# Kernel tuning notes

Measured on AMD Instinct MI355X. Metric: run time of the kernel, lower is better.

The kernel has to match this reference:

```python
import jax, jax.numpy as jnp
import numpy as np

B, S, D, E = 4, 1024, 1024, 4
HID = 2816  # multiple_of * ceil(int(2*4*D/3) / multiple_of), multiple_of=256
COND = 1024  # min(D, 1024)
NORM_EPS = 1e-5  # block norms
LN_EPS = 1e-5    # q_norm/k_norm default eps


def setup_inputs() -> dict:
    key = jax.random.key(0)
    ks = jax.random.split(key, 16)
    w = lambda i, shape: jax.random.normal(ks[i], shape, jnp.float32) * 0.02
    return {
        'x': jax.random.normal(ks[0], (B, S, D), jnp.float32),
        'freqs_cis': jax.random.normal(ks[1], (S, 32), jnp.float32),  # unused by the block
        'adaln_input': jax.random.normal(ks[2], (B, COND), jnp.float32),
        'wq': w(3, (D, D)), 'wk': w(4, (D, D)), 'wv': w(5, (D, D)), 'wo': w(6, (D, D)),
        'q_norm_w': jnp.ones((D,), jnp.float32), 'q_norm_b': jnp.zeros((D,), jnp.float32),
        'k_norm_w': jnp.ones((D,), jnp.float32), 'k_norm_b': jnp.zeros((D,), jnp.float32),
        'attn_norm_w': jnp.ones((D,), jnp.float32), 'attn_norm_b': jnp.zeros((D,), jnp.float32),
        'ffn_norm_w': jnp.ones((D,), jnp.float32), 'ffn_norm_b': jnp.zeros((D,), jnp.float32),
        'w1': w(7, (E, D, HID)), 'w2': w(8, (E, HID, D)), 'w3': w(9, (E, D, HID)),
        'router_w': w(10, (D, E)), 'router_b': jnp.zeros((E,), jnp.float32),
        'ada_w': w(11, (COND, 6 * D)), 'ada_b': jnp.zeros((6 * D,), jnp.float32),
    }


def _ln(x, w, b, eps):
    mu = jnp.mean(x, -1, keepdims=True)
    var = jnp.mean((x - mu) ** 2, -1, keepdims=True)
    return (x - mu) * jax.lax.rsqrt(var + eps) * w + b


def _attention(x, wq, wk, wv, wo, qn_w, qn_b, kn_w, kn_b):
    # NOTE: this module attends over the FEATURE dim (no head split, no 1/sqrt(d) scale):
    # xq,xk,xv are permuted to [B, D, S]; scores are [B, D, D].
    q = _ln(x @ wq, qn_w, qn_b, LN_EPS)
    k = _ln(x @ wk, kn_w, kn_b, LN_EPS)
    v = x @ wv
    scores = jnp.einsum('bsd,bse->bde', q, k)          # [B, D, D]
    attn = jax.nn.softmax(scores, axis=-1)
    out = jnp.einsum('bde,bse->bsd', attn, v)          # [B, S, D]
    return out @ wo


def _moe(x, w1, w2, w3, router_w, router_b):
    logits = x @ router_w + router_b                   # [B, S, E]
    # F.normalize default dim=1 -> L2-normalize along the SEQUENCE dim (faithful quirk)
    nrm = jnp.sqrt(jnp.sum(logits * logits, axis=1, keepdims=True))
    logits = logits / jnp.maximum(nrm, 1e-12)
    probs = jax.nn.softmax(logits, axis=-1)
    topw, topi = jax.lax.top_k(probs, 2)
    # dense combine weights [B,S,E]: identical math to the masked gather/scatter dispatch
    combine = jnp.sum(jax.nn.one_hot(topi, E, dtype=x.dtype) * topw[..., None], axis=-2)
    h1 = jnp.einsum('bsd,edh->ebsh', x, w1)
    h3 = jnp.einsum('bsd,edh->ebsh', x, w3)
    out_e = jnp.einsum('ebsh,ehd->ebsd', jnp.sin(h1) * h3, w2)
    moe = jnp.einsum('bse,ebsd->bsd', combine, out_e)
    avg = jnp.mean(probs, axis=0)                      # [S, E] (mean over batch dim only)
    aux = jnp.sum((1.0 / E - avg) ** 2)
    return moe, aux


def reference(x, freqs_cis, adaln_input, wq, wk, wv, wo, q_norm_w, q_norm_b, k_norm_w,
              k_norm_b, attn_norm_w, attn_norm_b, ffn_norm_w, ffn_norm_b, w1, w2, w3,
              router_w, router_b, ada_w, ada_b):
    ada = jax.nn.silu(adaln_input) @ ada_w + ada_b     # [B, 6D]
    shift_msa, scale_msa, gate_msa, shift_mlp, scale_mlp, gate_mlp = jnp.split(ada, 6, axis=1)
    h = _ln(x, attn_norm_w, attn_norm_b, NORM_EPS)
    h = h * (1.0 + scale_msa[:, None, :]) + shift_msa[:, None, :]
    x = x + gate_msa[:, None, :] * _attention(h, wq, wk, wv, wo, q_norm_w, q_norm_b, k_norm_w, k_norm_b)
    h = _ln(x, ffn_norm_w, ffn_norm_b, NORM_EPS)
    h = h * (1.0 + scale_mlp[:, None, :]) + shift_mlp[:, None, :]
    # MoE path REPLACES x (no residual, gate_mlp unused) — faithful to the source
    x, aux = _moe(h, w1, w2, w3, router_w, router_b)
    return x, aux
```

## Files before the change

### kernel.cpp

```cpp
#include <hip/hip_runtime.h>
#include <hip/hip_bf16.h>
#include <math.h>

#define BB 4
#define SS 1024
#define DD 1024
#define EE 4
#define HID 2816
#define HC 1408
#define SIXD 6144
#define NSLOT 8704
#define NMB 68

typedef __bf16 v8bf __attribute__((ext_vector_type(8)));
typedef float  v4f  __attribute__((ext_vector_type(4)));

__device__ __forceinline__ ushort f2bf(float f) {
    union { float f; unsigned u; } v; v.f = f;
    unsigned r = v.u + 0x7fff + ((v.u >> 16) & 1);
    return (ushort)(r >> 16);
}
__device__ __forceinline__ float bf2f(ushort u) {
    union { unsigned u; float f; } v; v.u = ((unsigned)u) << 16;
    return v.f;
}
__device__ __forceinline__ void split_bf(float x, ushort& h, ushort& l) {
    h = f2bf(x);
    l = f2bf(x - bf2f(h));
}
__device__ __forceinline__ void gload16(const void* g, void* l) {
    __builtin_amdgcn_global_load_lds((const __attribute__((address_space(1))) void*)g,
                                     (__attribute__((address_space(3))) void*)l, 16, 0, 0);
}
template<int N> __device__ __forceinline__ void wait_vm() {
    __builtin_amdgcn_s_waitcnt((N & 15) | (0x7 << 4) | (0xF << 8) | ((N >> 4) << 14));
}

__device__ __forceinline__ void xcd_remap(int& bx, int& by) {
    const int gx = gridDim.x, gy = gridDim.y;
    const int nwg = gx * gy;
    const int wid = bx + gx * by;
    const int q = nwg >> 3, r = nwg & 7;
    const int xcd = wid & 7, loc = wid >> 3;
    const int pos = (xcd < r) ? (xcd * (q + 1) + loc)
                              : (r * (q + 1) + (xcd - r) * q + loc);
    bx = pos % gx; by = pos / gx;
}

__device__ __forceinline__ void xcd_remap_cm(int& bx, int& by) {
    const int gx = gridDim.x, gy = gridDim.y;
    const int nwg = gx * gy;
    const int wid = bx + gx * by;
    const int q = nwg >> 3, r = nwg & 7;
    const int xcd = wid & 7, loc = wid >> 3;
    const int pos = (xcd < r) ? (xcd * (q + 1) + loc)
                              : (r * (q + 1) + (xcd - r) * q + loc);
    bx = pos / gy; by = pos % gy;
}

__device__ __forceinline__ void moe_remap(int& bx, int& by) {
    const int gx = gridDim.x, gy = gridDim.y;
    const int total = gx * gy;
    const int wid = bx + gx * by;
    if ((total & 7) || (gx & 1)) { xcd_remap(bx, by); return; }
    const int q = total >> 3;
    const int pos = (wid & 7) * q + (wid >> 3);
    const int NG = gx >> 1;
    const int gh = NG * gy;
    const int nh = pos / gh, r = pos % gh;
    by = r / NG;
    bx = nh * NG + (r % NG);
}

template<int EPI, bool SPLIT, bool MOE>
__global__ __launch_bounds__(256, 2) void mgemm(
    const ushort* __restrict__ Ah, const ushort* __restrict__ Al,
    const ushort* __restrict__ Bh, const ushort* __restrict__ Bl,
    void* __restrict__ Cv, ushort* __restrict__ C2,
    const float* __restrict__ f1, const float* __restrict__ f2,
    const int* __restrict__ tokidx, const int* __restrict__ mbe,
    const int* __restrict__ mbm,
    int K, int lda, int ldb, int ldc,
    long sA, long sB, long sC)
{
    constexpr int STG = SPLIT ? 12288 : 6144;
    constexpr int BH  = SPLIT ? 8192 : 4096;
    constexpr int L   = SPLIT ? 6 : 3;
    __shared__ __align__(16) ushort smem[3 * STG];

    const int tid  = threadIdx.x;
    const int wv   = tid >> 6, lane = tid & 63;

    int bx = blockIdx.x, by = blockIdx.y;
    if (MOE) moe_remap(bx, by); else xcd_remap(bx, by);
    const int n0 = bx * 64;

    int eexp = 0, m0;
    if (MOE) {
        eexp = mbe[by];
        if (eexp < 0) return;
        m0 = mbm[by];
    } else {
        m0 = by * 128;
    }
    const long zA = MOE ? 0 : (long)blockIdx.z * sA;
    const long zB = MOE ? (long)eexp * sB : (long)blockIdx.z * sB;
    const long zC = MOE ? 0 : (long)blockIdx.z * sC;

    const int lrow = tid >> 2;
    const int skq  = ((tid & 3) ^ ((tid >> 3) & 3)) * 8;
    const int lm   = lane & 15;
    const int qs   = (((lane >> 4) ^ ((lm >> 1) & 3)) * 8);

    v4f acc[2][4];
    const v4f vzero = {0.f, 0.f, 0.f, 0.f};
    #pragma unroll
    for (int i = 0; i < 2; ++i)
        #pragma unroll
        for (int j = 0; j < 4; ++j) acc[i][j] = vzero;

    auto issue = [&](int kt, int st) {
        const long kk = (long)kt * 32 + skq;
        ushort* base = smem + st * STG;
        #pragma unroll
        for (int c = 0; c < 2; ++c) {
            const int row  = c * 64 + lrow;
            const int loff = (c * 64 + wv * 16) * 32;
            gload16(Ah + zA + (long)(m0 + row) * lda + kk, base + loff);
            if (SPLIT)
                gload16(Al + zA + (long)(m0 + row) * lda + kk, base + 4096 + loff);
        }
        {
            const int loff = wv * 16 * 32;
            gload16(Bh + zB + (long)(n0 + lrow) * ldb + kk, base + BH + loff);
            if (SPLIT)
                gload16(Bl + zB + (long)(n0 + lrow) * ldb + kk, base + BH + 2048 + loff);
        }
    };

    const int nk = K / 32;
    issue(0, 0);
    if (nk > 1) issue(1, 1);
    for (int kt = 0; kt < nk; ++kt) {
        if (kt + 1 < nk) wait_vm<L>(); else wait_vm<0>();
        __builtin_amdgcn_s_barrier();
        if (kt + 2 < nk) issue(kt + 2, (kt + 2) % 3);
        const ushort* As = smem + (kt % 3) * STG;
        v8bf a[2], b[4];
        #pragma unroll
        for (int i = 0; i < 2; ++i) a[i] = *(const v8bf*)(As + (wv*32 + 16*i + lm) * 32 + qs);
        #pragma unroll
        for (int j = 0; j < 4; ++j) b[j] = *(const v8bf*)(As + BH + (16*j + lm) * 32 + qs);
        #pragma unroll
        for (int i = 0; i < 2; ++i)
            #pragma unroll
            for (int j = 0; j < 4; ++j)
                acc[i][j] = __builtin_amdgcn_mfma_f32_16x16x32_bf16(a[i], b[j], acc[i][j], 0, 0, 0);
        if (SPLIT) {
            v8bf al[2], bl[4];
            #pragma unroll
            for (int i = 0; i < 2; ++i) al[i] = *(const v8bf*)(As + 4096 + (wv*32 + 16*i + lm) * 32 + qs);
            #pragma unroll
            for (int j = 0; j < 4; ++j) bl[j] = *(const v8bf*)(As + BH + 2048 + (16*j + lm) * 32 + qs);
            #pragma unroll
            for (int i = 0; i < 2; ++i)
                #pragma unroll
                for (int j = 0; j < 4; ++j) {
                    acc[i][j] = __builtin_amdgcn_mfma_f32_16x16x32_bf16(a[i],  bl[j], acc[i][j], 0, 0, 0);
                    acc[i][j] = __builtin_amdgcn_mfma_f32_16x16x32_bf16(al[i], b[j],  acc[i][j], 0, 0, 0);
                }
        }
    }

    const int r0 = (lane >> 4) * 4;
    if (EPI == 7) {
        #pragma unroll
        for (int i = 0; i < 2; ++i)
            #pragma unroll
            for (int r = 0; r < 4; ++r) {
                const int rowg = m0 + wv*32 + 16*i + r0 + r;
                const int t = tokidx[rowg];
                if (t >= 0) {
                    const float cw = f1[t * 4 + eexp];
                    #pragma unroll
                    for (int j = 0; j < 4; ++j)
                        atomicAdd((float*)Cv + (long)t * 1024 + n0 + 16*j + lm, cw * acc[i][j][r]);
                }
            }
    } else {
        #pragma unroll
        for (int i = 0; i < 2; ++i) {
            #pragma unroll
            for (int j = 0; j < 4; ++j) {
                const int colg = n0 + 16*j + lm;
                #pragma unroll
                for (int r = 0; r < 4; ++r) {
                    const long rowg = (long)(m0 + wv*32 + 16*i + r0 + r);
                    const long idx  = zC + rowg * ldc + colg;
                    const float val = acc[i][j][r];
                    if (EPI == 0) {
                        ((float*)Cv)[idx] = val;
                    } else if (EPI == 2) {
                        ((float*)Cv)[idx] = f1[idx] + f2[(rowg >> 10) * SIXD + 2048 + colg] * val;
                    } else if (EPI == 5) {
                        ushort h, l; split_bf(val, h, l);
                        ((ushort*)Cv)[idx] = h;
                        C2[idx] = l;
                    }
                }
            }
        }
    }
}

__global__ __launch_bounds__(256, 2) void mgemm_qkv(
    const ushort* __restrict__ Ah, const ushort* __restrict__ Al,
    const ushort* __restrict__ Bqh, const ushort* __restrict__ Bql,
    const ushort* __restrict__ Bkh, const ushort* __restrict__ Bkl,
    const ushort* __restrict__ Bvh, const ushort* __restrict__ Bvl,
    float* __restrict__ Cq, float* __restrict__ Ck,
    ushort* __restrict__ Cvh, ushort* __restrict__ Cvl)
{
    constexpr int STG = 20480;
    __shared__ __align__(16) ushort smem[2 * STG];

    const int tid  = threadIdx.x;
    const int wv   = tid >> 6, lane = tid & 63;

    int bx = blockIdx.x, by = blockIdx.y;
    xcd_remap(bx, by);
    const int n0 = bx * 64, m0 = by * 128;

    const int lrow = tid >> 2;
    const int skq  = ((tid & 3) ^ ((tid >> 3) & 3)) * 8;
    const int lm   = lane & 15;
    const int qs   = (((lane >> 4) ^ ((lm >> 1) & 3)) * 8);

    const ushort* Bh_[3] = {Bqh, Bkh, Bvh};
    const ushort* Bl_[3] = {Bql, Bkl, Bvl};

    v4f aq[2][4], ak[2][4], av[2][4];
    const v4f vzero = {0.f, 0.f, 0.f, 0.f};
    #pragma unroll
    for (int i = 0; i < 2; ++i)
        #pragma unroll
        for (int j = 0; j < 4; ++j) { aq[i][j] = vzero; ak[i][j] = vzero; av[i][j] = vzero; }

    auto issue = [&](int kt, int st) {
        const long kk = (long)kt * 32 + skq;
        ushort* base = smem + st * STG;
        #pragma unroll
        for (int c = 0; c < 2; ++c) {
            const int row  = c * 64 + lrow;
            const int loff = (c * 64 + wv * 16) * 32;
            gload16(Ah + (long)(m0 + row) * 1024 + kk, base + loff);
            gload16(Al + (long)(m0 + row) * 1024 + kk, base + 4096 + loff);
        }
        const int loff = wv * 16 * 32;
        #pragma unroll
        for (int m = 0; m < 3; ++m) {
            gload16(Bh_[m] + (long)(n0 + lrow) * 1024 + kk, base + 8192 + m * 4096 + loff);
            gload16(Bl_[m] + (long)(n0 + lrow) * 1024 + kk, base + 8192 + m * 4096 + 2048 + loff);
        }
    };

    issue(0, 0);
    #pragma unroll 1
    for (int kt = 0; kt < 32; ++kt) {
        const int stg = kt & 1;
        if (kt) __builtin_amdgcn_s_barrier();
        const bool hasNext = (kt + 1 < 32);
        if (hasNext) issue(kt + 1, stg ^ 1);
        if (hasNext) wait_vm<10>(); else wait_vm<0>();
        __builtin_amdgcn_s_barrier();
        const ushort* As = smem + stg * STG;
        v8bf a[2], alo[2];
        #pragma unroll
        for (int i = 0; i < 2; ++i) {
            a[i]   = *(const v8bf*)(As + (wv*32 + 16*i + lm) * 32 + qs);
            alo[i] = *(const v8bf*)(As + 4096 + (wv*32 + 16*i + lm) * 32 + qs);
        }
        auto mat = [&](const ushort* Bs, v4f (&acc)[2][4]) {
            v8bf b[4], bl[4];
            #pragma unroll
            for (int j = 0; j < 4; ++j) {
                b[j]  = *(const v8bf*)(Bs + (16*j + lm) * 32 + qs);
                bl[j] = *(const v8bf*)(Bs + 2048 + (16*j + lm) * 32 + qs);
            }
            #pragma unroll
            for (int i = 0; i < 2; ++i)
                #pragma unroll
                for (int j = 0; j < 4; ++j) {
                    acc[i][j] = __builtin_amdgcn_mfma_f32_16x16x32_bf16(a[i],   b[j],  acc[i][j], 0, 0, 0);
                    acc[i][j] = __builtin_amdgcn_mfma_f32_16x16x32_bf16(a[i],   bl[j], acc[i][j], 0, 0, 0);
                    acc[i][j] = __builtin_amdgcn_mfma_f32_16x16x32_bf16(alo[i], b[j],  acc[i][j], 0, 0, 0);
                }
        };
        mat(As + 8192,        aq);
        mat(As + 8192 + 4096, ak);
        mat(As + 8192 + 8192, av);
    }

    const int r0 = (lane >> 4) * 4;
    #pragma unroll
    for (int i = 0; i < 2; ++i)
        #pragma unroll
        for (int j = 0; j < 4; ++j) {
            const int colg = n0 + 16*j + lm;
            #pragma unroll
            for (int r = 0; r < 4; ++r) {
                const long rowg = (long)(m0 + wv*32 + 16*i + r0 + r);
                const long idx  = rowg * 1024 + colg;
                Cq[idx] = aq[i][j][r];
                Ck[idx] = ak[i][j][r];
                ushort h, l; split_bf(av[i][j][r], h, l);
                Cvh[idx] = h;
                Cvl[idx] = l;
            }
        }
}

__global__ __launch_bounds__(512, 2) void mgemm_h1h3(
    const ushort* __restrict__ Ah, const ushort* __restrict__ B1,
    const ushort* __restrict__ B2, ushort* __restrict__ Cb,
    const int* __restrict__ tokidx, const int* __restrict__ mbe,
    const int* __restrict__ mbm, long sB)
{
    constexpr int STG = 12288;
    __shared__ __align__(16) ushort smem[3 * STG];

    const int tid  = threadIdx.x;
    const int wv   = tid >> 6, lane = tid & 63;
    const int wr   = wv >> 2, wc = wv & 3;

    int bx = blockIdx.x, by = blockIdx.y;
    xcd_remap_cm(bx, by);
    const int n0 = bx * 128;
    const int eexp = mbe[by];
    if (eexp < 0) return;
    const int m0 = mbm[by];
    const long zB = (long)eexp * sB;

    const int lrow = tid >> 2;
    const int skq  = ((tid & 3) ^ ((tid >> 3) & 3)) * 8;
    const int lm   = lane & 15;
    const int qs   = (((lane >> 4) ^ ((lm >> 1) & 3)) * 8);

    const int t = tokidx[m0 + lrow];
    const long arow = (t < 0) ? 0 : (long)t;

    v4f acc[4][2], acc2[4][2];
    const v4f vzero = {0.f, 0.f, 0.f, 0.f};
    #pragma unroll
    for (int i = 0; i < 4; ++i)
        #pragma unroll
        for (int j = 0; j < 2; ++j) { acc[i][j] = vzero; acc2[i][j] = vzero; }

    auto issue = [&](int kt, int st) {
        const long kk = (long)kt * 32 + skq;
        ushort* base = smem + st * STG;
        const int loff = wv * 16 * 32;
        gload16(Ah + arow * 1024 + kk, base + loff);
        gload16(B1 + zB + (long)(n0 + lrow) * 1024 + kk, base + 4096 + loff);
        gload16(B2 + zB + (long)(n0 + lrow) * 1024 + kk, base + 8192 + loff);
    };

    issue(0, 0);
    issue(1, 1);
    int s_cur = 0, s_nxt = 2;
    #pragma unroll 1
    for (int kt = 0; kt < 32; ++kt) {
        if (kt + 1 < 32) wait_vm<3>(); else wait_vm<0>();
        __builtin_amdgcn_s_barrier();
        if (kt + 2 < 32) issue(kt + 2, s_nxt);
        const ushort* As = smem + s_cur * STG;
        v8bf a[4], b1[2], b2[2];
        #pragma unroll
        for (int i = 0; i < 4; ++i) a[i] = *(const v8bf*)(As + (wr*64 + 16*i + lm) * 32 + qs);
        #pragma unroll
        for (int j = 0; j < 2; ++j) {
            b1[j] = *(const v8bf*)(As + 4096 + (wc*32 + 16*j + lm) * 32 + qs);
            b2[j] = *(const v8bf*)(As + 8192 + (wc*32 + 16*j + lm) * 32 + qs);
        }
        #pragma unroll
        for (int i = 0; i < 4; ++i)
            #pragma unroll
            for (int j = 0; j < 2; ++j) {
                acc[i][j]  = __builtin_amdgcn_mfma_f32_16x16x32_bf16(a[i], b1[j], acc[i][j],  0, 0, 0);
                acc2[i][j] = __builtin_amdgcn_mfma_f32_16x16x32_bf16(a[i], b2[j], acc2[i][j], 0, 0, 0);
            }
        s_cur = (s_cur == 2) ? 0 : s_cur + 1;
        s_nxt = (s_nxt == 2) ? 0 : s_nxt + 1;
    }

    const int r0 = (lane >> 4) * 4;
    #pragma unroll
    for (int i = 0; i < 4; ++i)
        #pragma unroll
        for (int j = 0; j < 2; ++j) {
            const int colg = n0 + wc*32 + 16*j + lm;
            #pragma unroll
            for (int r = 0; r < 4; ++r) {
                const long rowg = (long)(m0 + wr*64 + 16*i + r0 + r);
                Cb[rowg * HC + colg] = f2bf(sinf(acc[i][j][r]) * acc2[i][j][r]);
            }
        }
}

template<bool SP>
__global__ __launch_bounds__(256) void transp(
    const float* __restrict__ in, ushort* __restrict__ oh, ushort* __restrict__ ol,
    int ldin, int ldout, long sIn, long sOut)
{
    __shared__ float T[64][65];
    const int n0 = blockIdx.x * 64, k0 = blockIdx.y * 64;
    in += (long)blockIdx.z * sIn;
    oh += (long)blockIdx.z * sOut;
    if (SP) ol += (long)blockIdx.z * sOut;
    const int t = threadIdx.x;
    const int rr = t >> 4, c4 = (t & 15) * 4;
    #pragma unroll
    for (int p = 0; p < 4; ++p) {
        const int r = rr + p * 16;
        const float4 v = *(const float4*)(in + (long)(k0 + r) * ldin + n0 + c4);
        T[c4+0][r] = v.x; T[c4+1][r] = v.y; T[c4+2][r] = v.z; T[c4+3][r] = v.w;
    }
    __syncthreads();
    #pragma unroll
    for (int p = 0; p < 4; ++p) {
        const int idx = t + 256 * p;
        const int n = idx >> 4, c = (idx & 15) * 4;
        ushort4 wh, wl;
        float x0 = T[n][c], x1 = T[n][c+1], x2 = T[n][c+2], x3 = T[n][c+3];
        if (SP) {
            split_bf(x0, wh.x, wl.x); split_bf(x1, wh.y, wl.y);
            split_bf(x2, wh.z, wl.z); split_bf(x3, wh.w, wl.w);
        } else {
            wh.x = f2bf(x0); wh.y = f2bf(x1); wh.z = f2bf(x2); wh.w = f2bf(x3);
        }
        *(ushort4*)(oh + (long)(n0 + n) * ldout + k0 + c) = wh;
        if (SP) *(ushort4*)(ol + (long)(n0 + n) * ldout + k0 + c) = wl;
    }
}

__global__ __launch_bounds__(256) void ada_kernel(
    const float* __restrict__ adaln, const float* __restrict__ aw,
    const float* __restrict__ ab, float* __restrict__ ada)
{
    __shared__ float s[DD];
    const int b = blockIdx.y;
    const int tid = threadIdx.x;
    for (int i = tid; i < DD; i += 256) {
        const float v = adaln[(long)b * DD + i];
        s[i] = v / (1.f + expf(-v));
    }
    __syncthreads();
    const int n = blockIdx.x * 256 + tid;
    float acc = 0.f;
    for (int k = 0; k < DD; ++k) acc += s[k] * aw[(long)k * SIXD + n];
    ada[(long)b * SIXD + n] = acc + ab[n];
}

template<int OUT, bool MOD>
__global__ __launch_bounds__(256) void ln_kernel(
    const float* __restrict__ x, const float* __restrict__ w, const float* __restrict__ bias,
    const float* __restrict__ ada, int scale_off, int shift_off,
    float* __restrict__ o32, ushort* __restrict__ oh, ushort* __restrict__ ol, float eps)
{
    const int row = blockIdx.x;
    const int b = row >> 10;
    const int tid = threadIdx.x;
    const float* xr = x + (long)row * DD;
    float v[4]; float s = 0.f, q = 0.f;
    #pragma unroll
    for (int i = 0; i < 4; ++i) { v[i] = xr[tid + 256*i]; s += v[i]; q += v[i]*v[i]; }
    __shared__ float rs_[256], rq_[256];
    rs_[tid] = s; rq_[tid] = q; __syncthreads();
    for (int off = 128; off > 0; off >>= 1) {
        if (tid < off) { rs_[tid] += rs_[tid+off]; rq_[tid] += rq_[tid+off]; }
        __syncthreads();
    }
    const float mu  = rs_[0] * (1.f/DD);
    const float var = rq_[0] * (1.f/DD) - mu*mu;
    const float rstd = rsqrtf(var + eps);
    const float* ar = ada + (long)b * SIXD;
    #pragma unroll
    for (int i = 0; i < 4; ++i) {
        const int d = tid + 256*i;
        float y = (v[i] - mu) * rstd * w[d] + bias[d];
        if (MOD) y = y * (1.f + ar[scale_off + d]) + ar[shift_off + d];
        const long idx = (long)row * DD + d;
        if (OUT == 0) o32[idx] = y;
        else if (OUT == 1) { ushort h, l; split_bf(y, h, l); oh[idx] = h; ol[idx] = l; }
        else oh[idx] = f2bf(y);
    }
}

__global__ __launch_bounds__(256) void softmax_split(
    const float* __restrict__ in, ushort* __restrict__ oh, ushort* __restrict__ ol)
{
    const long row = blockIdx.x;
    const float* p = in + row * 1024;
    const int tid = threadIdx.x;
    float v[4]; float mx = -INFINITY;
    #pragma unroll
    for (int i = 0; i < 4; ++i) { v[i] = p[tid + 256*i]; mx = fmaxf(mx, v[i]); }
    __shared__ float red[256];
    red[tid] = mx; __syncthreads();
    for (int off = 128; off > 0; off >>= 1) {
        if (tid < off) red[tid] = fmaxf(red[tid], red[tid+off]);
        __syncthreads();
    }
    const float rowmax = red[0];
    __syncthreads();
    float s = 0.f;
    #pragma unroll
    for (int i = 0; i < 4; ++i) { v[i] = expf(v[i] - rowmax); s += v[i]; }
    red[tid] = s; __syncthreads();
    for (int off = 128; off > 0; off >>= 1) {
        if (tid < off) red[tid] += red[tid+off];
        __syncthreads();
    }
    const float inv = 1.f / red[0];
    #pragma unroll
    for (int i = 0; i < 4; ++i) {
        ushort h, l; split_bf(v[i] * inv, h, l);
        oh[row*1024 + tid + 256*i] = h;
        ol[row*1024 + tid + 256*i] = l;
    }
}

__global__ __launch_bounds__(256) void router_fused(
    const float* __restrict__ x2, const float* __restrict__ fw, const float* __restrict__ fb,
    const float* __restrict__ ada, const float* __restrict__ rw, const float* __restrict__ rb,
    float* __restrict__ logits)
{
    const int row = blockIdx.x;
    const int b = row >> 10;
    const int tid = threadIdx.x;
    const float* xr = x2 + (long)row * DD;
    float v[4]; float s = 0.f, q = 0.f;
    #pragma unroll
    for (int i = 0; i < 4; ++i) { v[i] = xr[tid + 256*i]; s += v[i]; q += v[i]*v[i]; }
    __shared__ float rs_[256], rq_[256];
    rs_[tid] = s; rq_[tid] = q; __syncthreads();
    for (int off = 128; off > 0; off >>= 1) {
        if (tid < off) { rs_[tid] += rs_[tid+off]; rq_[tid] += rq_[tid+off]; }
        __syncthreads();
    }
    const float mu  = rs_[0] * (1.f/DD);
    const float var = rq_[0] * (1.f/DD) - mu*mu;
    const float rstd = rsqrtf(var + 1e-5f);
    const float* ar = ada + (long)b * SIXD;
    float acc[4] = {0.f, 0.f, 0.f, 0.f};
    #pragma unroll
    for (int i = 0; i < 4; ++i) {
        const int d = tid + 256*i;
        float h = (v[i] - mu) * rstd * fw[d] + fb[d];
        h = h * (1.f + ar[4096 + d]) + ar[3072 + d];
        const float* r4 = rw + (long)d * 4;
        acc[0] += h*r4[0]; acc[1] += h*r4[1]; acc[2] += h*r4[2]; acc[3] += h*r4[3];
    }
    __syncthreads();
    __shared__ float red[256];
    for (int e = 0; e < EE; ++e) {
        red[tid] = acc[e]; __syncthreads();
        for (int off = 128; off > 0; off >>= 1) {
            if (tid < off) red[tid] += red[tid+off];
            __syncthreads();
        }
        if (tid == 0) logits[(long)row * EE + e] = red[0] + rb[e];
        __syncthreads();
    }
}

__global__ __launch_bounds__(1024) void router_all(
    const float* __restrict__ logits, float* __restrict__ comb,
    float* __restrict__ auxout, int* __restrict__ tokidx,
    int* __restrict__ mbe, int* __restrict__ mbm)
{
    __shared__ float pl[16384];
    __shared__ float red[1024];
    __shared__ float nrm_l[16];
    __shared__ int lc[4], loff[4], lpos[4];
    const int tid = threadIdx.x;
    const int wv = tid >> 6, ln = tid & 63;
    {
        const int b = wv >> 2, e = wv & 3;
        float s = 0.f;
        for (int it = 0; it < 16; ++it) {
            const float v = logits[(((long)b << 10) + ln + (it << 6)) * 4 + e];
            s += v * v;
        }
        for (int off = 32; off > 0; off >>= 1) s += __shfl_down(s, off, 64);
        if (ln == 0) nrm_l[wv] = fmaxf(sqrtf(s), 1e-12f);
    }
    if (tid < 4) lc[tid] = 0;
    __syncthreads();
    float cloc[4][4];
    const int rbase = tid * 4;
    for (int rr = 0; rr < 4; ++rr) {
        const int row = rbase + rr;
        const int b = row >> 10;
        float l[4], p[4];
        #pragma unroll
        for (int e = 0; e < 4; ++e) l[e] = logits[(long)row*4 + e] / nrm_l[b*4 + e];
        const float mx = fmaxf(fmaxf(l[0], l[1]), fmaxf(l[2], l[3]));
        float s = 0.f;
        #pragma unroll
        for (int e = 0; e < 4; ++e) { p[e] = expf(l[e] - mx); s += p[e]; }
        const float inv = 1.f / s;
        #pragma unroll
        for (int e = 0; e < 4; ++e) { p[e] *= inv; pl[row*4 + e] = p[e]; }
        int i1 = 0;
        #pragma unroll
        for (int e = 1; e < 4; ++e) if (p[e] > p[i1]) i1 = e;
        int i2 = (i1 == 0) ? 1 : 0;
        #pragma unroll
        for (int e = 0; e < 4; ++e) if (e != i1 && p[e] > p[i2]) i2 = e;
        #pragma unroll
        for (int e = 0; e < 4; ++e) {
            const float c = (e == i1) ? p[i1] : ((e == i2) ? p[i2] : 0.f);
            cloc[rr][e] = c;
            comb[(long)row*4 + e] = c;
            if (c > 0.f) atomicAdd(&lc[e], 1);
        }
    }
    __syncthreads();
    float acc = 0.f;
    for (int i = tid; i < 4096; i += 1024) {
        const int s = i >> 2, e = i & 3;
        const float avg = 0.25f * (pl[s*4+e] + pl[(1024+s)*4+e] +
                                   pl[(2048+s)*4+e] + pl[(3072+s)*4+e]);
        const float d = 0.25f - avg;
        acc += d * d;
    }
    red[tid] = acc; __syncthreads();
    for (int off = 512; off > 0; off >>= 1) {
        if (tid < off) red[tid] += red[tid+off];
        __syncthreads();
    }
    if (tid == 0) auxout[0] = red[0];
    if (tid == 0) {
        int off0 = 0, nb = 0;
        for (int e = 0; e < 4; ++e) {
            loff[e] = off0; lpos[e] = 0;
            const int mb = (lc[e] + 127) >> 7;
            for (int k = 0; k < mb; ++k) { mbe[nb] = e; mbm[nb] = off0 + k*128; ++nb; }
            off0 += mb << 7;
        }
        for (; nb < NMB; ++nb) { mbe[nb] = -1; mbm[nb] = 0; }
    }
    for (int i = tid; i < NSLOT; i += 1024) tokidx[i] = -1;
    __syncthreads();
    for (int rr = 0; rr < 4; ++rr) {
        const int row = rbase + rr;
        #pragma unroll
        for (int e = 0; e < 4; ++e)
            if (cloc[rr][e] > 0.f) {
                const int s = atomicAdd(&lpos[e], 1);
                tokidx[loff[e] + s] = row;
            }
    }
}

__global__ __launch_bounds__(256) void zero_kernel(float4* __restrict__ out)
{
    out[(long)blockIdx.x * 256 + threadIdx.x] = float4{0.f, 0.f, 0.f, 0.f};
}

extern "C" void kernel_launch(void* const* d_in, const int* in_sizes, int n_in,
                              void* d_out, int out_size, void* d_ws, size_t ws_size,
                              hipStream_t stream)
{
    (void)in_sizes; (void)n_in; (void)out_size; (void)ws_size;
    const float* x     = (const float*)d_in[0];
    const float* adaln = (const float*)d_in[2];
    const float* wq    = (const float*)d_in[3];
    const float* wk    = (const float*)d_in[4];
    const float* wv    = (const float*)d_in[5];
    const float* wo    = (const float*)d_in[6];
    const float* qn_w  = (const float*)d_in[7];
    const float* qn_b  = (const float*)d_in[8];
    const float* kn_w  = (const float*)d_in[9];
    const float* kn_b  = (const float*)d_in[10];
    const float* an_w  = (const float*)d_in[11];
    const float* an_b  = (const float*)d_in[12];
    const float* fn_w  = (const float*)d_in[13];
    const float* fn_b  = (const float*)d_in[14];
    const float* w1    = (const float*)d_in[15];
    const float* w2    = (const float*)d_in[16];
    const float* w3    = (const float*)d_in[17];
    const float* rw    = (const float*)d_in[18];
    const float* rb    = (const float*)d_in[19];
    const float* aw    = (const float*)d_in[20];
    const float* ab    = (const float*)d_in[21];
    float* out = (float*)d_out;

    const long NBAT = (long)SS * DD;
    const long NBUF = (long)BB * SS * DD;
#define MB(x) ((long)(x) * 1048576L)

    char* P = (char*)d_ws;
    float* ada    = (float*)P;
    float* logits = (float*)(P + 98304);
    float* comb   = logits + 16384;
    int*   tokidx = (int*)(comb + 16384);
    int*   mbe    = tokidx + NSLOT;
    int*   mbm    = mbe + NMB;

    char* A0 = P + MB(1);
    ushort* wqT_h = (ushort*)(A0 + MB(0));  ushort* wqT_l = (ushort*)(A0 + MB(2));
    ushort* wkT_h = (ushort*)(A0 + MB(4));  ushort* wkT_l = (ushort*)(A0 + MB(6));
    ushort* wvT_h = (ushort*)(A0 + MB(8));  ushort* wvT_l = (ushort*)(A0 + MB(10));
    ushort* woT_h = (ushort*)(A0 + MB(0));  ushort* woT_l = (ushort*)(A0 + MB(2));
    ushort* w1Tc  = (ushort*)(A0 + MB(0));
    ushort* h_h   = (ushort*)(A0 + MB(12)); ushort* h_l  = (ushort*)(A0 + MB(20));
    ushort* qT_h  = (ushort*)(A0 + MB(12)); ushort* qT_l = (ushort*)(A0 + MB(20));
    ushort* ao_h  = (ushort*)(A0 + MB(12)); ushort* ao_l = (ushort*)(A0 + MB(20));
    ushort* actb  = (ushort*)(A0 + MB(12));
    float*  q32   = (float*) (A0 + MB(28));
    float*  sc    = (float*) (A0 + MB(28));
    float*  x2    = (float*) (A0 + MB(28));
    ushort* v_h   = (ushort*)(A0 + MB(44)); ushort* v_l  = (ushort*)(A0 + MB(52));
    float*  k32   = (float*) (A0 + MB(60));
    ushort* at_h  = (ushort*)(A0 + MB(60)); ushort* at_l = (ushort*)(A0 + MB(68));
    ushort* w3Tc  = (ushort*)(A0 + MB(60));
    ushort* kT_h  = (ushort*)(A0 + MB(76)); ushort* kT_l = (ushort*)(A0 + MB(84));
    ushort* h2bf  = (ushort*)(A0 + MB(76));
    ushort* w2Tc  = (ushort*)(A0 + MB(84));

    const dim3 blk(256);

    ada_kernel<<<dim3(SIXD/256, BB), blk, 0, stream>>>(adaln, aw, ab, ada);

    transp<true><<<dim3(16,16,1), blk, 0, stream>>>(wq, wqT_h, wqT_l, 1024, 1024, 0, 0);
    transp<true><<<dim3(16,16,1), blk, 0, stream>>>(wk, wkT_h, wkT_l, 1024, 1024, 0, 0);
    transp<true><<<dim3(16,16,1), blk, 0, stream>>>(wv, wvT_h, wvT_l, 1024, 1024, 0, 0);

    ln_kernel<1,true><<<4096, blk, 0, stream>>>(x, an_w, an_b, ada, 1024, 0,
                                                nullptr, h_h, h_l, 1e-5f);

    mgemm_qkv<<<dim3(16,32), blk, 0, stream>>>(
        h_h, h_l, wqT_h, wqT_l, wkT_h, wkT_l, wvT_h, wvT_l,
        q32, k32, v_h, v_l);

    ln_kernel<0,false><<<4096, blk, 0, stream>>>(q32, qn_w, qn_b, ada, 0, 0, q32, nullptr, nullptr, 1e-5f);
    transp<true><<<dim3(16,16,BB), blk, 0, stream>>>(q32, qT_h, qT_l, 1024, 1024, NBAT, NBAT);

    ln_kernel<0,false><<<4096, blk, 0, stream>>>(k32, kn_w, kn_b, ada, 0, 0, k32, nullptr, nullptr, 1e-5f);
    transp<true><<<dim3(16,16,BB), blk, 0, stream>>>(k32, kT_h, kT_l, 1024, 1024, NBAT, NBAT);

    transp<true><<<dim3(16,16,1), blk, 0, stream>>>(wo, woT_h, woT_l, 1024, 1024, 0, 0);

    mgemm<0,true,false><<<dim3(16,8,BB), blk, 0, stream>>>(
        qT_h, qT_l, kT_h, kT_l, sc, nullptr, nullptr, nullptr, nullptr, nullptr, nullptr,
        1024, 1024, 1024, 1024, NBAT, NBAT, NBAT);

    softmax_split<<<4096, blk, 0, stream>>>(sc, at_h, at_l);

    mgemm<5,true,false><<<dim3(16,8,BB), blk, 0, stream>>>(
        v_h, v_l, at_h, at_l, ao_h, ao_l, nullptr, nullptr, nullptr, nullptr, nullptr,
        1024, 1024, 1024, 1024, NBAT, NBAT, NBAT);

    mgemm<2,true,false><<<dim3(16,32,1), blk, 0, stream>>>(
        ao_h, ao_l, woT_h, woT_l, x2, nullptr, x, ada, nullptr, nullptr, nullptr,
        1024, 1024, 1024, 1024, 0, 0, 0);

    ln_kernel<2,true><<<4096, blk, 0, stream>>>(x2, fn_w, fn_b, ada, 4096, 3072,
                                                nullptr, h2bf, nullptr, 1e-5f);

    router_fused<<<4096, blk, 0, stream>>>(x2, fn_w, fn_b, ada, rw, rb, logits);
    router_all<<<1, dim3(1024), 0, stream>>>(logits, comb, out + NBUF, tokidx, mbe, mbm);
    zero_kernel<<<dim3(4096), blk, 0, stream>>>((float4*)out);

    for (int c = 0; c < HID/HC; ++c) {
        transp<false><<<dim3(22,16,4), blk, 0, stream>>>(
            w1 + (long)c*HC, w1Tc, nullptr, HID, 1024, (long)DD*HID, (long)HC*1024);
        transp<false><<<dim3(22,16,4), blk, 0, stream>>>(
            w3 + (long)c*HC, w3Tc, nullptr, HID, 1024, (long)DD*HID, (long)HC*1024);
        transp<false><<<dim3(16,22,4), blk, 0, stream>>>(
            w2 + (long)c*HC*DD, w2Tc, nullptr, DD, HC, (long)HID*DD, (long)DD*HC);
        mgemm_h1h3<<<dim3(11, NMB), dim3(512), 0, stream>>>(
            h2bf, w1Tc, w3Tc, actb, tokidx, mbe, mbm, (long)HC*1024);
        mgemm<7,false,true><<<dim3(16, NMB), blk, 0, stream>>>(
            actb, nullptr, w2Tc, nullptr, out, nullptr, comb, nullptr, tokidx, mbe, mbm,
            HC, HC, HC, 1024, 0, (long)DD*HC, 0);
    }
#undef MB
}
```

Measured before the change: 794.9 us.

## Enlarge MoE h1/h3 GEMM tile to 256 rows and fuse FFN norm into router

The fused w1/w3 expert GEMM now uses 256-row by 128-column tiles with 8 waves laid out 4x2, each wave holding a 64x64 output. Per-expert token padding is now 256-aligned, so NSLOT and the microblock counts grow and a second block list (mbe2/mbm2) is built for the larger tiles. This is meant to improve weight reuse and the MFMA-to-load ratio. In exchange it uses more LDS and registers, drops to one block per CU, and adds more padding rows. Separately, the FFN layernorm's bf16 output is written from the router kernel, which removes one pass over x2.

New measurement: 917.5 us. 15.4% more time.

```diff
diff --git a/kernel.cpp b/kernel.cpp
--- a/kernel.cpp
+++ b/kernel.cpp
@@ -9,8 +9,9 @@
 #define HID 2816
 #define HC 1408
 #define SIXD 6144
-#define NSLOT 8704
-#define NMB 68
+#define NSLOT 9216
+#define NMB 80
+#define NMB2 40
 
 typedef __bf16 v8bf __attribute__((ext_vector_type(8)));
 typedef float  v4f  __attribute__((ext_vector_type(4)));
@@ -320,25 +321,25 @@
         }
 }
 
-__global__ __launch_bounds__(512, 2) void mgemm_h1h3(
+__global__ __launch_bounds__(512, 1) void mgemm_h1h3(
     const ushort* __restrict__ Ah, const ushort* __restrict__ B1,
     const ushort* __restrict__ B2, ushort* __restrict__ Cb,
-    const int* __restrict__ tokidx, const int* __restrict__ mbe,
-    const int* __restrict__ mbm, long sB)
-{
-    constexpr int STG = 12288;
+    const int* __restrict__ tokidx, const int* __restrict__ mbe2,
+    const int* __restrict__ mbm2, long sB)
+{
+    constexpr int STG = 16384;
     __shared__ __align__(16) ushort smem[3 * STG];
 
     const int tid  = threadIdx.x;
     const int wv   = tid >> 6, lane = tid & 63;
-    const int wr   = wv >> 2, wc = wv & 3;
+    const int wr   = wv >> 1, wc = wv & 1;
 
     int bx = blockIdx.x, by = blockIdx.y;
     xcd_remap_cm(bx, by);
     const int n0 = bx * 128;
-    const int eexp = mbe[by];
+    const int eexp = mbe2[by];
     if (eexp < 0) return;
-    const int m0 = mbm[by];
+    const int m0 = mbm2[by];
     const long zB = (long)eexp * sB;
 
     const int lrow = tid >> 2;
@@ -346,23 +347,28 @@
     const int lm   = lane & 15;
     const int qs   = (((lane >> 4) ^ ((lm >> 1) & 3)) * 8);
 
-    const int t = tokidx[m0 + lrow];
-    const long arow = (t < 0) ? 0 : (long)t;
-
-    v4f acc[4][2], acc2[4][2];
+    long arow[2];
+    #pragma unroll
+    for (int c = 0; c < 2; ++c) {
+        const int t = tokidx[m0 + c * 128 + lrow];
+        arow[c] = (t < 0) ? 0 : (long)t;
+    }
+
+    v4f acc[4][4], acc2[4][4];
     const v4f vzero = {0.f, 0.f, 0.f, 0.f};
     #pragma unroll
     for (int i = 0; i < 4; ++i)
         #pragma unroll
-        for (int j = 0; j < 2; ++j) { acc[i][j] = vzero; acc2[i][j] = vzero; }
+        for (int j = 0; j < 4; ++j) { acc[i][j] = vzero; acc2[i][j] = vzero; }
 
     auto issue = [&](int kt, int st) {
         const long kk = (long)kt * 32 + skq;
         ushort* base = smem + st * STG;
-        const int loff = wv * 16 * 32;
-        gload16(Ah + arow * 1024 + kk, base + loff);
-        gload16(B1 + zB + (long)(n0 + lrow) * 1024 + kk, base + 4096 + loff);
-        gload16(B2 + zB + (long)(n0 + lrow) * 1024 + kk, base + 8192 + loff);
+        #pragma unroll
+        for (int c = 0; c < 2; ++c)
+            gload16(Ah + arow[c] * 1024 + kk, base + c * 4096 + tid * 8);
+        gload16(B1 + zB + (long)(n0 + lrow) * 1024 + kk, base + 8192 + tid * 8);
+        gload16(B2 + zB + (long)(n0 + lrow) * 1024 + kk, base + 12288 + tid * 8);
     };
 
     issue(0, 0);
@@ -370,22 +376,22 @@
     int s_cur = 0, s_nxt = 2;
     #pragma unroll 1
     for (int kt = 0; kt < 32; ++kt) {
-        if (kt + 1 < 32) wait_vm<3>(); else wait_vm<0>();
+        if (kt + 1 < 32) wait_vm<4>(); else wait_vm<0>();
         __builtin_amdgcn_s_barrier();
         if (kt + 2 < 32) issue(kt + 2, s_nxt);
         const ushort* As = smem + s_cur * STG;
-        v8bf a[4], b1[2], b2[2];
+        v8bf a[4], b1[4], b2[4];
         #pragma unroll
         for (int i = 0; i < 4; ++i) a[i] = *(const v8bf*)(As + (wr*64 + 16*i + lm) * 32 + qs);
         #pragma unroll
-        for (int j = 0; j < 2; ++j) {
-            b1[j] = *(const v8bf*)(As + 4096 + (wc*32 + 16*j + lm) * 32 + qs);
-            b2[j] = *(const v8bf*)(As + 8192 + (wc*32 + 16*j + lm) * 32 + qs);
+        for (int j = 0; j < 4; ++j) {
+            b1[j] = *(const v8bf*)(As + 8192 + (wc*64 + 16*j + lm) * 32 + qs);
+            b2[j] = *(const v8bf*)(As + 12288 + (wc*64 + 16*j + lm) * 32 + qs);
         }
         #pragma unroll
         for (int i = 0; i < 4; ++i)
             #pragma unroll
-            for (int j = 0; j < 2; ++j) {
+            for (int j = 0; j < 4; ++j) {
                 acc[i][j]  = __builtin_amdgcn_mfma_f32_16x16x32_bf16(a[i], b1[j], acc[i][j],  0, 0, 0);
                 acc2[i][j] = __builtin_amdgcn_mfma_f32_16x16x32_bf16(a[i], b2[j], acc2[i][j], 0, 0, 0);
             }
@@ -397,8 +403,8 @@
     #pragma unroll
     for (int i = 0; i < 4; ++i)
         #pragma unroll
-        for (int j = 0; j < 2; ++j) {
-            const int colg = n0 + wc*32 + 16*j + lm;
+        for (int j = 0; j < 4; ++j) {
+            const int colg = n0 + wc*64 + 16*j + lm;
             #pragma unroll
             for (int r = 0; r < 4; ++r) {
                 const long rowg = (long)(m0 + wr*64 + 16*i + r0 + r);
@@ -530,10 +536,10 @@
     }
 }
 
-__global__ __launch_bounds__(256) void router_fused(
+__global__ __launch_bounds__(256) void ln_router(
     const float* __restrict__ x2, const float* __restrict__ fw, const float* __restrict__ fb,
     const float* __restrict__ ada, const float* __restrict__ rw, const float* __restrict__ rb,
-    float* __restrict__ logits)
+    float* __restrict__ logits, ushort* __restrict__ oh)
 {
     const int row = blockIdx.x;
     const int b = row >> 10;
@@ -558,6 +564,7 @@
         const int d = tid + 256*i;
         float h = (v[i] - mu) * rstd * fw[d] + fb[d];
         h = h * (1.f + ar[4096 + d]) + ar[3072 + d];
+        oh[(long)row * DD + d] = f2bf(h);
         const float* r4 = rw + (long)d * 4;
         acc[0] += h*r4[0]; acc[1] += h*r4[1]; acc[2] += h*r4[2]; acc[3] += h*r4[3];
     }
@@ -577,7 +584,8 @@
 __global__ __launch_bounds__(1024) void router_all(
     const float* __restrict__ logits, float* __restrict__ comb,
     float* __restrict__ auxout, int* __restrict__ tokidx,
-    int* __restrict__ mbe, int* __restrict__ mbm)
+    int* __restrict__ mbe, int* __restrict__ mbm,
+    int* __restrict__ mbe2, int* __restrict__ mbm2)
 {
     __shared__ float pl[16384];
     __shared__ float red[1024];
@@ -642,14 +650,16 @@
     }
     if (tid == 0) auxout[0] = red[0];
     if (tid == 0) {
-        int off0 = 0, nb = 0;
+        int off0 = 0, nb = 0, nb2 = 0;
         for (int e = 0; e < 4; ++e) {
             loff[e] = off0; lpos[e] = 0;
-            const int mb = (lc[e] + 127) >> 7;
-            for (int k = 0; k < mb; ++k) { mbe[nb] = e; mbm[nb] = off0 + k*128; ++nb; }
-            off0 += mb << 7;
-        }
-        for (; nb < NMB; ++nb) { mbe[nb] = -1; mbm[nb] = 0; }
+            const int mb2c = (lc[e] + 255) >> 8;
+            for (int k = 0; k < 2*mb2c; ++k) { mbe[nb] = e; mbm[nb] = off0 + k*128; ++nb; }
+            for (int k = 0; k < mb2c;   ++k) { mbe2[nb2] = e; mbm2[nb2] = off0 + k*256; ++nb2; }
+            off0 += mb2c << 8;
+        }
+        for (; nb < NMB; ++nb)   { mbe[nb] = -1;  mbm[nb] = 0; }
+        for (; nb2 < NMB2; ++nb2){ mbe2[nb2] = -1; mbm2[nb2] = 0; }
     }
     for (int i = tid; i < NSLOT; i += 1024) tokidx[i] = -1;
     __syncthreads();
@@ -708,6 +718,8 @@
     int*   tokidx = (int*)(comb + 16384);
     int*   mbe    = tokidx + NSLOT;
     int*   mbm    = mbe + NMB;
+    int*   mbe2   = mbm + NMB;
+    int*   mbm2   = mbe2 + NMB2;
 
     char* A0 = P + MB(1);
     ushort* wqT_h = (ushort*)(A0 + MB(0));  ushort* wqT_l = (ushort*)(A0 + MB(2));
@@ -767,11 +779,10 @@
         ao_h, ao_l, woT_h, woT_l, x2, nullptr, x, ada, nullptr, nullptr, nullptr,
         1024, 1024, 1024, 1024, 0, 0, 0);
 
-    ln_kernel<2,true><<<4096, blk, 0, stream>>>(x2, fn_w, fn_b, ada, 4096, 3072,
-                                                nullptr, h2bf, nullptr, 1e-5f);
-
-    router_fused<<<4096, blk, 0, stream>>>(x2, fn_w, fn_b, ada, rw, rb, logits);
-    router_all<<<1, dim3(1024), 0, stream>>>(logits, comb, out + NBUF, tokidx, mbe, mbm);
+    ln_router<<<4096, blk, 0, stream>>>(x2, fn_w, fn_b, ada, rw, rb, logits, h2bf);
+
+    router_all<<<1, dim3(1024), 0, stream>>>(logits, comb, out + NBUF, tokidx,
+                                             mbe, mbm, mbe2, mbm2);
     zero_kernel<<<dim3(4096), blk, 0, stream>>>((float4*)out);
 
     for (int c = 0; c < HID/HC; ++c) {
@@ -781,8 +792,8 @@
             w3 + (long)c*HC, w3Tc, nullptr, HID, 1024, (long)DD*HID, (long)HC*1024);
         transp<false><<<dim3(16,22,4), blk, 0, stream>>>(
             w2 + (long)c*HC*DD, w2Tc, nullptr, DD, HC, (long)HID*DD, (long)DD*HC);
-        mgemm_h1h3<<<dim3(11, NMB), dim3(512), 0, stream>>>(
-            h2bf, w1Tc, w3Tc, actb, tokidx, mbe, mbm, (long)HC*1024);
+        mgemm_h1h3<<<dim3(11, NMB2), dim3(512), 0, stream>>>(
+            h2bf, w1Tc, w3Tc, actb, tokidx, mbe2, mbm2, (long)HC*1024);
         mgemm<7,false,true><<<dim3(16, NMB), blk, 0, stream>>>(
             actb, nullptr, w2Tc, nullptr, out, nullptr, comb, nullptr, tokidx, mbe, mbm,
             HC, HC, HC, 1024, 0, (long)DD*HC, 0);
```
